# Kernel optimization log

Measured on AMD Instinct MI355X. Metric: run time of the kernel, lower is better.

The kernel has to match this reference:

```python
import jax, jax.numpy as jnp
import numpy as np

D_MODEL, N_GROUPS, N_EXPERTS = 512, 8, 8
TOP_K_L1, TOP_K_L2 = 2, 2
BATCH, SEQ = 2, 512


def setup_inputs() -> dict:
    key = jax.random.key(0)
    ks = jax.random.split(key, 6)
    d, G, E = D_MODEL, N_GROUPS, N_EXPERTS
    scale = 0.02
    x = jax.random.normal(ks[0], (BATCH, SEQ, d), dtype=jnp.float32)
    g1 = jax.random.normal(ks[1], (d, G), dtype=jnp.float32) * scale          # level-1 gate (no bias)
    g2 = jax.random.normal(ks[2], (G, d, E), dtype=jnp.float32) * scale       # per-group level-2 gate (no bias)
    W1 = jax.random.normal(ks[3], (G, E, d, 2 * d), dtype=jnp.float32) * scale
    b1 = jnp.zeros((G, E, 2 * d), dtype=jnp.float32)
    W2 = jax.random.normal(ks[4], (G, E, 2 * d, d), dtype=jnp.float32) * scale
    b2 = jnp.zeros((G, E, d), dtype=jnp.float32)
    return {"x": x, "g1": g1, "g2": g2, "W1": W1, "b1": b1, "W2": W2, "b2": b2}


def reference(x, g1, g2, W1, b1, W2, b2):
    B, S, d = x.shape
    G, E = g1.shape[1], g2.shape[2]
    xt = x.reshape(-1, d)  # [T, d]

    # ---- level-1 routing (groups) ----
    logits1 = xt @ g1                                   # [T, G]
    v1, i1 = jax.lax.top_k(logits1, TOP_K_L1)           # [T, k1]
    w1 = jax.nn.softmax(v1.astype(jnp.float32), axis=-1).astype(x.dtype)
    # dense combine weights: top-k indices are unique per token, so one-hot sum
    # is exactly the original gather/index_add_ math.
    c1 = jnp.sum(jax.nn.one_hot(i1, G, dtype=x.dtype) * w1[..., None], axis=1)  # [T, G]

    # ---- level-2 routing (experts within each group) ----
    logits2 = jnp.einsum('td,gde->tge', xt, g2)         # [T, G, E]
    v2, i2 = jax.lax.top_k(logits2, TOP_K_L2)           # [T, G, k2]
    w2 = jax.nn.softmax(v2.astype(jnp.float32), axis=-1).astype(x.dtype)
    c2 = jnp.sum(jax.nn.one_hot(i2, E, dtype=x.dtype) * w2[..., None], axis=2)  # [T, G, E]

    # ---- expert MLPs (Linear -> ReLU -> Linear), all experts, combined by weights ----
    h = jax.nn.relu(jnp.einsum('td,gedh->tgeh', xt, W1) + b1)   # [T, G, E, 2d]
    y = jnp.einsum('tgeh,gehd->tged', h, W2) + b2               # [T, G, E, d]

    group_out = jnp.einsum('tged,tge->tgd', y, c2)              # level-2 combine
    out = jnp.einsum('tgd,tg->td', group_out, c1)               # level-1 combine
    return out.reshape(B, S, d)
```

## Files before the change

kernel.cpp:

```cpp
#include <hip/hip_runtime.h>
#include <hip/hip_bf16.h>

#define D_M   512
#define H_M   1024
#define G_N   8
#define E_N   8
#define T_N   1024
#define NEXP  64
#define CAP   1024

#define LDK   520

typedef __attribute__((ext_vector_type(8))) short bf16x8;
typedef __attribute__((ext_vector_type(4))) float f32x4;
typedef __attribute__((ext_vector_type(4))) unsigned int u32x4;

__device__ __forceinline__ unsigned short f2bf(float f) {
  unsigned u = __builtin_bit_cast(unsigned, f);
  u = (u + 0x7fffu + ((u >> 16) & 1u)) >> 16;
  return (unsigned short)u;
}
__device__ __forceinline__ unsigned pack2(float a, float b) {
  return (unsigned)f2bf(a) | ((unsigned)f2bf(b) << 16);
}

__global__ __launch_bounds__(64) void k_route(
    const float* __restrict__ x, const float* __restrict__ g1,
    const float* __restrict__ g2, int* __restrict__ slotGE,
    float* __restrict__ slotW) {
  __shared__ float xs[D_M];
  __shared__ float l2s[G_N][E_N];
  __shared__ float l1s[G_N];
  __shared__ float l1part[G_N][8];
  const int t = blockIdx.x;
  const int lane = threadIdx.x;
  const float* xr = x + (size_t)t * D_M;
  for (int i = lane; i < D_M; i += 64) xs[i] = xr[i];
  __syncthreads();
  {
    const int g = lane >> 3, e = lane & 7;
    const float* gp = g2 + (size_t)g * D_M * E_N + e;
    float acc = 0.f;
    #pragma unroll 8
    for (int i = 0; i < D_M; i++) acc += xs[i] * gp[(size_t)i * E_N];
    l2s[g][e] = acc;
  }
  {
    const int g = lane >> 3, c = lane & 7;
    float acc = 0.f;
    #pragma unroll 8
    for (int i = c * 64; i < c * 64 + 64; i++) acc += xs[i] * g1[(size_t)i * G_N + g];
    l1part[g][c] = acc;
  }
  __syncthreads();
  if (lane < G_N) {
    float s = 0.f;
    #pragma unroll
    for (int c = 0; c < 8; c++) s += l1part[lane][c];
    l1s[lane] = s;
  }
  __syncthreads();
  if (lane == 0) {
    int a1 = 0;
    for (int g = 1; g < G_N; g++) if (l1s[g] > l1s[a1]) a1 = g;
    int a2 = (a1 == 0) ? 1 : 0;
    for (int g = 0; g < G_N; g++) if (g != a1 && l1s[g] > l1s[a2]) a2 = g;
    const float m = l1s[a1];
    float w1a = __expf(l1s[a1] - m), w1b = __expf(l1s[a2] - m);
    const float inv = 1.f / (w1a + w1b);
    w1a *= inv; w1b *= inv;
    const int gsel[2] = {a1, a2};
    const float wsel[2] = {w1a, w1b};
    for (int a = 0; a < 2; a++) {
      const int g = gsel[a];
      int e1 = 0;
      for (int e = 1; e < E_N; e++) if (l2s[g][e] > l2s[g][e1]) e1 = e;
      int e2 = (e1 == 0) ? 1 : 0;
      for (int e = 0; e < E_N; e++) if (e != e1 && l2s[g][e] > l2s[g][e2]) e2 = e;
      const float mm = l2s[g][e1];
      float ua = __expf(l2s[g][e1] - mm), ub = __expf(l2s[g][e2] - mm);
      const float uin = 1.f / (ua + ub);
      ua *= uin; ub *= uin;
      slotGE[t * 4 + a * 2 + 0] = g * E_N + e1;
      slotW [t * 4 + a * 2 + 0] = wsel[a] * ua;
      slotGE[t * 4 + a * 2 + 1] = g * E_N + e2;
      slotW [t * 4 + a * 2 + 1] = wsel[a] * ub;
    }
  }
}

__global__ __launch_bounds__(256) void k_build(
    const int* __restrict__ slotGE, int* __restrict__ counts,
    int* __restrict__ list) {
  const int ts = blockIdx.x * 256 + threadIdx.x;
  if (ts >= T_N * 4) return;
  const int ge = slotGE[ts];
  const int pos = atomicAdd(&counts[ge], 1);
  list[ge * CAP + pos] = ts;
}

__global__ __launch_bounds__(256, 2) void k_mlp1(
    const float* __restrict__ x, const float* __restrict__ W1,
    const float* __restrict__ b1, const int* __restrict__ counts,
    const int* __restrict__ list, unsigned short* __restrict__ h_ws) {
  const int ge = blockIdx.x >> 3;
  const int j0 = (blockIdx.x & 7) * 128;
  const int n = counts[ge];
  if (n == 0) return;
  __shared__ unsigned short xl[64 * LDK];
  __shared__ int tokTS[64];
  const int tid = threadIdx.x;
  const int lane = tid & 63, wave = tid >> 6;
  const int m16 = lane & 15, quad = lane >> 4;

  const float* Wcol = W1 + (size_t)ge * (D_M * H_M) + j0 + wave * 32 + m16;
  float bv[2];
  #pragma unroll
  for (int nt = 0; nt < 2; nt++) bv[nt] = b1[ge * H_M + j0 + wave * 32 + nt * 16 + m16];

  for (int t0 = 0; t0 < n; t0 += 64) {
    __syncthreads();
    if (tid < 64) {
      int idx = t0 + tid;
      tokTS[tid] = list[ge * CAP + (idx < n ? idx : n - 1)];
    }
    __syncthreads();
    {
      const int trow = tid >> 2;
      const int kb = (tid & 3) * 4;
      const float* xr = x + (size_t)(tokTS[trow] >> 2) * D_M + kb;
      unsigned short* dst = &xl[trow * LDK + kb];
      #pragma unroll 8
      for (int rep = 0; rep < 32; rep++) {
        f32x4 v = *(const f32x4*)(xr + rep * 16);
        uint2 p = { pack2(v.x, v.y), pack2(v.z, v.w) };
        *(uint2*)(dst + rep * 16) = p;
      }
    }
    __syncthreads();

    f32x4 acc[4][2] = {};
    float bcur[2][8], bnxt[2][8];
    #pragma unroll
    for (int nt = 0; nt < 2; nt++)
      #pragma unroll
      for (int i = 0; i < 8; i++)
        bcur[nt][i] = Wcol[(size_t)(quad * 8 + i) * H_M + nt * 16];

    #pragma unroll 4
    for (int s = 0; s < 16; s++) {
      if (s < 15) {
        #pragma unroll
        for (int nt = 0; nt < 2; nt++)
          #pragma unroll
          for (int i = 0; i < 8; i++)
            bnxt[nt][i] = Wcol[(size_t)((s + 1) * 32 + quad * 8 + i) * H_M + nt * 16];
      }
      bf16x8 bf[2];
      #pragma unroll
      for (int nt = 0; nt < 2; nt++) {
        u32x4 t = { pack2(bcur[nt][0], bcur[nt][1]), pack2(bcur[nt][2], bcur[nt][3]),
                    pack2(bcur[nt][4], bcur[nt][5]), pack2(bcur[nt][6], bcur[nt][7]) };
        bf[nt] = __builtin_bit_cast(bf16x8, t);
      }
      #pragma unroll
      for (int mt = 0; mt < 4; mt++) {
        bf16x8 af = *(bf16x8*)&xl[(mt * 16 + m16) * LDK + s * 32 + quad * 8];
        acc[mt][0] = __builtin_amdgcn_mfma_f32_16x16x32_bf16(af, bf[0], acc[mt][0], 0, 0, 0);
        acc[mt][1] = __builtin_amdgcn_mfma_f32_16x16x32_bf16(af, bf[1], acc[mt][1], 0, 0, 0);
      }
      #pragma unroll
      for (int nt = 0; nt < 2; nt++)
        #pragma unroll
        for (int i = 0; i < 8; i++) bcur[nt][i] = bnxt[nt][i];
    }
    #pragma unroll
    for (int mt = 0; mt < 4; mt++)
      #pragma unroll
      for (int i = 0; i < 4; i++) {
        const int tr = mt * 16 + quad * 4 + i;
        if (t0 + tr < n) {
          const int ts = tokTS[tr];
          unsigned short* hp = h_ws + (size_t)ts * H_M + j0 + wave * 32 + m16;
          #pragma unroll
          for (int nt = 0; nt < 2; nt++) {
            float v = acc[mt][nt][i] + bv[nt];
            hp[nt * 16] = f2bf(v > 0.f ? v : 0.f);
          }
        }
      }
  }
}

__global__ __launch_bounds__(256, 2) void k_mlp2(
    const unsigned short* __restrict__ h_ws, const float* __restrict__ W2,
    const float* __restrict__ b2, const int* __restrict__ counts,
    const int* __restrict__ list, float* __restrict__ y0,
    float* __restrict__ y1) {
  const int ge = blockIdx.x >> 3;
  const int j0 = ((blockIdx.x >> 1) & 3) * 128;
  const int ks = blockIdx.x & 1;
  const int n = counts[ge];
  if (n == 0) return;
  __shared__ unsigned short xl[64 * LDK];
  __shared__ int tokTS[64];
  const int tid = threadIdx.x;
  const int lane = tid & 63, wave = tid >> 6;
  const int m16 = lane & 15, quad = lane >> 4;

  const float* Wcol = W2 + (size_t)ge * (H_M * D_M) + (size_t)(ks * 512) * D_M + j0 + wave * 32 + m16;
  float bv[2];
  #pragma unroll
  for (int nt = 0; nt < 2; nt++)
    bv[nt] = ks == 0 ? b2[ge * D_M + j0 + wave * 32 + nt * 16 + m16] : 0.f;
  float* yk = ks == 0 ? y0 : y1;

  for (int t0 = 0; t0 < n; t0 += 64) {
    __syncthreads();
    if (tid < 64) {
      int idx = t0 + tid;
      tokTS[tid] = list[ge * CAP + (idx < n ? idx : n - 1)];
    }
    __syncthreads();
    {
      const int trow = tid >> 2;
      const int kb = (tid & 3) * 8;
      const unsigned short* hr = h_ws + (size_t)tokTS[trow] * H_M + ks * 512 + kb;
      unsigned short* dst = &xl[trow * LDK + kb];
      #pragma unroll 8
      for (int rep = 0; rep < 16; rep++)
        *(u32x4*)(dst + rep * 32) = *(const u32x4*)(hr + rep * 32);
    }
    __syncthreads();

    f32x4 acc[4][2] = {};
    float bcur[2][8], bnxt[2][8];
    #pragma unroll
    for (int nt = 0; nt < 2; nt++)
      #pragma unroll
      for (int i = 0; i < 8; i++)
        bcur[nt][i] = Wcol[(size_t)(quad * 8 + i) * D_M + nt * 16];

    #pragma unroll 4
    for (int s = 0; s < 16; s++) {
      if (s < 15) {
        #pragma unroll
        for (int nt = 0; nt < 2; nt++)
          #pragma unroll
          for (int i = 0; i < 8; i++)
            bnxt[nt][i] = Wcol[(size_t)((s + 1) * 32 + quad * 8 + i) * D_M + nt * 16];
      }
      bf16x8 bf[2];
      #pragma unroll
      for (int nt = 0; nt < 2; nt++) {
        u32x4 t = { pack2(bcur[nt][0], bcur[nt][1]), pack2(bcur[nt][2], bcur[nt][3]),
                    pack2(bcur[nt][4], bcur[nt][5]), pack2(bcur[nt][6], bcur[nt][7]) };
        bf[nt] = __builtin_bit_cast(bf16x8, t);
      }
      #pragma unroll
      for (int mt = 0; mt < 4; mt++) {
        bf16x8 af = *(bf16x8*)&xl[(mt * 16 + m16) * LDK + s * 32 + quad * 8];
        acc[mt][0] = __builtin_amdgcn_mfma_f32_16x16x32_bf16(af, bf[0], acc[mt][0], 0, 0, 0);
        acc[mt][1] = __builtin_amdgcn_mfma_f32_16x16x32_bf16(af, bf[1], acc[mt][1], 0, 0, 0);
      }
      #pragma unroll
      for (int nt = 0; nt < 2; nt++)
        #pragma unroll
        for (int i = 0; i < 8; i++) bcur[nt][i] = bnxt[nt][i];
    }
    #pragma unroll
    for (int mt = 0; mt < 4; mt++)
      #pragma unroll
      for (int i = 0; i < 4; i++) {
        const int tr = mt * 16 + quad * 4 + i;
        if (t0 + tr < n) {
          const int ts = tokTS[tr];
          float* yp = yk + (size_t)ts * D_M + j0 + wave * 32 + m16;
          #pragma unroll
          for (int nt = 0; nt < 2; nt++)
            yp[nt * 16] = acc[mt][nt][i] + bv[nt];
        }
      }
  }
}

__global__ __launch_bounds__(256) void k_combine(
    const float* __restrict__ y0, const float* __restrict__ y1,
    const float* __restrict__ slotW, float* __restrict__ out) {
  const int idx = blockIdx.x * 256 + threadIdx.x;
  if (idx >= T_N * D_M / 4) return;
  const int t = idx >> 7;
  const int j = (idx & 127) * 4;
  float4 r = {0.f, 0.f, 0.f, 0.f};
  #pragma unroll
  for (int s = 0; s < 4; s++) {
    const float w = slotW[t * 4 + s];
    const size_t off = (size_t)(t * 4 + s) * D_M + j;
    const float4 a = *(const float4*)(y0 + off);
    const float4 b = *(const float4*)(y1 + off);
    r.x += w * (a.x + b.x);
    r.y += w * (a.y + b.y);
    r.z += w * (a.z + b.z);
    r.w += w * (a.w + b.w);
  }
  *(float4*)&out[(size_t)t * D_M + j] = r;
}

extern "C" void kernel_launch(void* const* d_in, const int* in_sizes, int n_in,
                              void* d_out, int out_size, void* d_ws, size_t ws_size,
                              hipStream_t stream) {
  const float* x  = (const float*)d_in[0];
  const float* g1 = (const float*)d_in[1];
  const float* g2 = (const float*)d_in[2];
  const float* W1 = (const float*)d_in[3];
  const float* b1 = (const float*)d_in[4];
  const float* W2 = (const float*)d_in[5];
  const float* b2 = (const float*)d_in[6];
  float* out = (float*)d_out;

  char* ws = (char*)d_ws;
  int*            slotGE = (int*)(ws + 0);
  float*          slotW  = (float*)(ws + 16384);
  int*            counts = (int*)(ws + 32768);
  int*            list   = (int*)(ws + 36864);
  unsigned short* h_ws   = (unsigned short*)(ws + 524288);
  float*          y0     = (float*)(ws + 524288 + 8388608);
  float*          y1     = (float*)(ws + 524288 + 16777216);

  hipMemsetAsync(counts, 0, NEXP * sizeof(int), stream);
  k_route<<<T_N, 64, 0, stream>>>(x, g1, g2, slotGE, slotW);
  k_build<<<(T_N * 4) / 256, 256, 0, stream>>>(slotGE, counts, list);
  k_mlp1<<<NEXP * 8, 256, 0, stream>>>(x, W1, b1, counts, list, h_ws);
  k_mlp2<<<NEXP * 8, 256, 0, stream>>>(h_ws, W2, b2, counts, list, y0, y1);
  k_combine<<<(T_N * D_M / 4) / 256, 256, 0, stream>>>(y0, y1, slotW, out);
}
```

Before: 372.6 us.

## Fuse token-list build into routing and split expert MLP tokens across blocks

Removes the separate k_build kernel by doing the per-expert atomic list append directly inside k_route. The two expert MLP kernels now also split each expert's token range four ways across blocks (grid grows 4x), so more blocks run in parallel when experts receive few tokens. The bf16 pack helper switches to the v_cvt_pk_bf16_f32 hardware instruction. The trade-off is that each block streams its weight column slice on its own, so weights are re-read across the token splits, and list order becomes nondeterministic.

```diff
diff --git a/kernel.cpp b/kernel.cpp
--- a/kernel.cpp
+++ b/kernel.cpp
@@ -15,19 +15,21 @@
 typedef __attribute__((ext_vector_type(4))) float f32x4;
 typedef __attribute__((ext_vector_type(4))) unsigned int u32x4;
 
+__device__ __forceinline__ unsigned pack2(float a, float b) {
+  unsigned r;
+  asm("v_cvt_pk_bf16_f32 %0, %1, %2" : "=v"(r) : "v"(a), "v"(b));
+  return r;
+}
 __device__ __forceinline__ unsigned short f2bf(float f) {
   unsigned u = __builtin_bit_cast(unsigned, f);
   u = (u + 0x7fffu + ((u >> 16) & 1u)) >> 16;
   return (unsigned short)u;
 }
-__device__ __forceinline__ unsigned pack2(float a, float b) {
-  return (unsigned)f2bf(a) | ((unsigned)f2bf(b) << 16);
-}
 
 __global__ __launch_bounds__(64) void k_route(
     const float* __restrict__ x, const float* __restrict__ g1,
-    const float* __restrict__ g2, int* __restrict__ slotGE,
-    float* __restrict__ slotW) {
+    const float* __restrict__ g2, float* __restrict__ slotW,
+    int* __restrict__ counts, int* __restrict__ list) {
   __shared__ float xs[D_M];
   __shared__ float l2s[G_N][E_N];
   __shared__ float l1s[G_N];
@@ -81,32 +83,28 @@
       float ua = __expf(l2s[g][e1] - mm), ub = __expf(l2s[g][e2] - mm);
       const float uin = 1.f / (ua + ub);
       ua *= uin; ub *= uin;
-      slotGE[t * 4 + a * 2 + 0] = g * E_N + e1;
-      slotW [t * 4 + a * 2 + 0] = wsel[a] * ua;
-      slotGE[t * 4 + a * 2 + 1] = g * E_N + e2;
-      slotW [t * 4 + a * 2 + 1] = wsel[a] * ub;
-    }
-  }
-}
-
-__global__ __launch_bounds__(256) void k_build(
-    const int* __restrict__ slotGE, int* __restrict__ counts,
-    int* __restrict__ list) {
-  const int ts = blockIdx.x * 256 + threadIdx.x;
-  if (ts >= T_N * 4) return;
-  const int ge = slotGE[ts];
-  const int pos = atomicAdd(&counts[ge], 1);
-  list[ge * CAP + pos] = ts;
+      const int ge0 = g * E_N + e1;
+      const int ge1 = g * E_N + e2;
+      slotW[t * 4 + a * 2 + 0] = wsel[a] * ua;
+      slotW[t * 4 + a * 2 + 1] = wsel[a] * ub;
+      int p0 = atomicAdd(&counts[ge0], 1);
+      list[ge0 * CAP + p0] = t * 4 + a * 2 + 0;
+      int p1 = atomicAdd(&counts[ge1], 1);
+      list[ge1 * CAP + p1] = t * 4 + a * 2 + 1;
+    }
+  }
 }
 
 __global__ __launch_bounds__(256, 2) void k_mlp1(
     const float* __restrict__ x, const float* __restrict__ W1,
     const float* __restrict__ b1, const int* __restrict__ counts,
     const int* __restrict__ list, unsigned short* __restrict__ h_ws) {
-  const int ge = blockIdx.x >> 3;
-  const int j0 = (blockIdx.x & 7) * 128;
+  const int bx = blockIdx.x;
+  const int ge = bx >> 5;
+  const int j0 = ((bx >> 2) & 7) * 128;
+  const int tt = bx & 3;
   const int n = counts[ge];
-  if (n == 0) return;
+  if (tt * 64 >= n) return;
   __shared__ unsigned short xl[64 * LDK];
   __shared__ int tokTS[64];
   const int tid = threadIdx.x;
@@ -118,7 +116,7 @@
   #pragma unroll
   for (int nt = 0; nt < 2; nt++) bv[nt] = b1[ge * H_M + j0 + wave * 32 + nt * 16 + m16];
 
-  for (int t0 = 0; t0 < n; t0 += 64) {
+  for (int t0 = tt * 64; t0 < n; t0 += 256) {
     __syncthreads();
     if (tid < 64) {
       int idx = t0 + tid;
@@ -197,11 +195,13 @@
     const float* __restrict__ b2, const int* __restrict__ counts,
     const int* __restrict__ list, float* __restrict__ y0,
     float* __restrict__ y1) {
-  const int ge = blockIdx.x >> 3;
-  const int j0 = ((blockIdx.x >> 1) & 3) * 128;
-  const int ks = blockIdx.x & 1;
+  const int bx = blockIdx.x;
+  const int ge = bx >> 5;
+  const int j0 = ((bx >> 3) & 3) * 128;
+  const int ks = (bx >> 2) & 1;
+  const int tt = bx & 3;
   const int n = counts[ge];
-  if (n == 0) return;
+  if (tt * 64 >= n) return;
   __shared__ unsigned short xl[64 * LDK];
   __shared__ int tokTS[64];
   const int tid = threadIdx.x;
@@ -215,7 +215,7 @@
     bv[nt] = ks == 0 ? b2[ge * D_M + j0 + wave * 32 + nt * 16 + m16] : 0.f;
   float* yk = ks == 0 ? y0 : y1;
 
-  for (int t0 = 0; t0 < n; t0 += 64) {
+  for (int t0 = tt * 64; t0 < n; t0 += 256) {
     __syncthreads();
     if (tid < 64) {
       int idx = t0 + tid;
@@ -319,7 +319,6 @@
   float* out = (float*)d_out;
 
   char* ws = (char*)d_ws;
-  int*            slotGE = (int*)(ws + 0);
   float*          slotW  = (float*)(ws + 16384);
   int*            counts = (int*)(ws + 32768);
   int*            list   = (int*)(ws + 36864);
@@ -328,9 +327,8 @@
   float*          y1     = (float*)(ws + 524288 + 16777216);
 
   hipMemsetAsync(counts, 0, NEXP * sizeof(int), stream);
-  k_route<<<T_N, 64, 0, stream>>>(x, g1, g2, slotGE, slotW);
-  k_build<<<(T_N * 4) / 256, 256, 0, stream>>>(slotGE, counts, list);
-  k_mlp1<<<NEXP * 8, 256, 0, stream>>>(x, W1, b1, counts, list, h_ws);
-  k_mlp2<<<NEXP * 8, 256, 0, stream>>>(h_ws, W2, b2, counts, list, y0, y1);
+  k_route<<<T_N, 64, 0, stream>>>(x, g1, g2, slotW, counts, list);
+  k_mlp1<<<NEXP * 32, 256, 0, stream>>>(x, W1, b1, counts, list, h_ws);
+  k_mlp2<<<NEXP * 32, 256, 0, stream>>>(h_ws, W2, b2, counts, list, y0, y1);
   k_combine<<<(T_N * D_M / 4) / 256, 256, 0, stream>>>(y0, y1, slotW, out);
 }
```

Result: slower. 431.3 us (+15.7%).
